# Kernel optimization log

Measured on AMD Instinct MI355X. Metric: run time of the kernel, lower is better.

The kernel has to match this reference:

```python
import jax, jax.numpy as jnp
import numpy as np

N, E, B, T, F, H, O = 50000, 800000, 16, 4, 128, 128, 128
LEAKY = 0.2  # PyG GATConv negative_slope default


def setup_inputs() -> dict:
    key = jax.random.key(0)
    ks = jax.random.split(key, 12)
    s = 0.05
    return {
        "x": jax.random.normal(ks[0], (T, N, F), jnp.float32),
        "edge_index": jax.random.randint(ks[1], (2, E), 0, N, dtype=jnp.int32),
        "batch_idx": jnp.sort(jax.random.randint(ks[2], (N,), 0, B, dtype=jnp.int32)),
        "W1": jax.random.normal(ks[3], (F, H), jnp.float32) * s,
        "att_src1": jax.random.normal(ks[4], (H,), jnp.float32) * s,
        "att_dst1": jax.random.normal(ks[5], (H,), jnp.float32) * s,
        "b1": jnp.zeros((H,), jnp.float32),
        "W2": jax.random.normal(ks[6], (H, O), jnp.float32) * s,
        "att_src2": jax.random.normal(ks[7], (O,), jnp.float32) * s,
        "att_dst2": jax.random.normal(ks[8], (O,), jnp.float32) * s,
        "b2": jnp.zeros((O,), jnp.float32),
    }


def gat_layer(h, src, dst, W, a_src, a_dst, b):
    # PyG GATConv, heads=1, concat=False, self-loops already appended.
    h = h @ W                                  # [N, out]
    alpha_s = h @ a_src                        # [N]
    alpha_d = h @ a_dst                        # [N]
    e = alpha_s[src] + alpha_d[dst]            # [E']
    e = jnp.where(e > 0, e, LEAKY * e)         # leaky_relu
    # softmax over incoming edges of each destination node (every node has a self-loop)
    m = jax.ops.segment_max(e, dst, num_segments=N)
    ex = jnp.exp(e - m[dst])
    z = jax.ops.segment_sum(ex, dst, num_segments=N)
    alpha = ex / z[dst]                        # [E']
    out = jax.ops.segment_sum(alpha[:, None] * h[src], dst, num_segments=N)
    return out + b


def reference(x, edge_index, batch_idx, W1, att_src1, att_dst1, b1, W2, att_src2, att_dst2, b2):
    loops = jnp.arange(N, dtype=edge_index.dtype)
    src = jnp.concatenate([edge_index[0], loops])  # add_self_loops (PyG default)
    dst = jnp.concatenate([edge_index[1], loops])
    ones = jnp.ones((N, 1), jnp.float32)
    cnt = jax.ops.segment_sum(ones, batch_idx, num_segments=B)  # [B,1]

    def per_snapshot(xt):
        h = gat_layer(xt, src, dst, W1, att_src1, att_dst1, b1)
        h = jax.nn.relu(h)                     # inter-layer ReLU (dropout=0, eval)
        h = gat_layer(h, src, dst, W2, att_src2, att_dst2, b2)
        return jax.ops.segment_sum(h, batch_idx, num_segments=B) / cnt  # mean pool [B,O]

    reps = jax.vmap(per_snapshot)(x)           # [T, B, O]
    return jnp.transpose(reps, (1, 0, 2))      # [B, T, O]
```

## Files before the change

kernel.cpp:

```cpp
#include <hip/hip_runtime.h>
#include <hip/hip_bf16.h>

#define LEAKY 0.2f

typedef __attribute__((ext_vector_type(8))) short bf16x8;
typedef __attribute__((ext_vector_type(4))) float f32x4;
typedef __attribute__((ext_vector_type(2))) float f32x2;


__global__ __launch_bounds__(256) void k_init(int* cnt, int* bstart, int* hist, int n, int nb) {
    int i = blockIdx.x * 256 + threadIdx.x;
    if (i < n) cnt[i] = 1;
    if (i < nb) bstart[i] = n;
    if (i < 32) hist[i] = 0;
}

__global__ __launch_bounds__(256) void k_count(const int* __restrict__ dst, int* cnt, int e,
                                               const int* __restrict__ bidx, int* bstart, int n) {
    int i = blockIdx.x * 256 + threadIdx.x;
    if (i < e) atomicAdd(&cnt[dst[i]], 1);
    if (i < n) {
        int b = bidx[i];
        if (i == 0 || bidx[i - 1] != b) atomicMin(&bstart[b], i);
    }
}

__device__ inline int block_incl_scan(int v, int* lds) {
    int lane = threadIdx.x & 63, wid = threadIdx.x >> 6;
    int s = v;
#pragma unroll
    for (int o = 1; o < 64; o <<= 1) { int t = __shfl_up(s, o); if (lane >= o) s += t; }
    if (lane == 63) lds[wid] = s;
    __syncthreads();
    int add = 0;
#pragma unroll
    for (int ww = 0; ww < 3; ++ww) if (ww < wid) add += lds[ww];
    return s + add;
}

__global__ __launch_bounds__(256) void k_scanA(const int* __restrict__ cnt, int* bsum, int n) {
    __shared__ int lds[4];
    int i = blockIdx.x * 256 + threadIdx.x;
    int v = (i < n) ? ((cnt[i] + 15) & ~15) : 0;
    int s = block_incl_scan(v, lds);
    if (threadIdx.x == 255) bsum[blockIdx.x] = s;
}

__global__ __launch_bounds__(256) void k_scanB(int* bsum, int* boff, int nb,
                                               int* bstart, int n, int nbatch) {
    __shared__ int lds[4];
    int i = threadIdx.x;
    int v = (i < nb) ? bsum[i] : 0;
    int s = block_incl_scan(v, lds);
    if (i < nb) boff[i] = s - v;
    if (i == 0) {
        bstart[nbatch] = n;
        for (int b = nbatch - 1; b >= 0; --b)
            if (bstart[b] == n) bstart[b] = bstart[b + 1];
    }
}

__global__ __launch_bounds__(256) void k_scanC(const int* __restrict__ cnt, const int* __restrict__ boff,
                                               int* row_ptr, int* csr, int* cursor, int* hist, int n) {
    __shared__ int lds[4];
    __shared__ int lh[32];
    int tid = threadIdx.x;
    if (tid < 32) lh[tid] = 0;
    int i = blockIdx.x * 256 + tid;
    int v = (i < n) ? ((cnt[i] + 15) & ~15) : 0;
    int s = block_incl_scan(v, lds) + boff[blockIdx.x];
    __syncthreads();
    if (i < n) {
        int excl = s - v;
        row_ptr[i + 1] = s;
        csr[excl] = i;
        cursor[i] = excl + 1;
        atomicAdd(&lh[min(v >> 4, 31)], 1);
    }
    if (i == 0) row_ptr[0] = 0;
    __syncthreads();
    if (tid < 32 && lh[tid]) atomicAdd(&hist[tid], lh[tid]);
}

__global__ __launch_bounds__(256) void k_scatter(const int* __restrict__ src, const int* __restrict__ dst,
                                                 int* cursor, int* csr, int e) {
    int i = blockIdx.x * 256 + threadIdx.x;
    if (i < e) { int p = atomicAdd(&cursor[dst[i]], 1); csr[p] = src[i]; }
}

__global__ void k_bscan(const int* __restrict__ hist, int* bcur) {
    int run = 0;
    for (int b = 0; b < 32; ++b) { bcur[b] = run; run += hist[b]; }
}

__global__ __launch_bounds__(256) void k_pad(const int* __restrict__ row_ptr, const int* __restrict__ cursor,
                                             int* csr, int* bcur, int* perm, int n) {
    __shared__ int lh[32];
    __shared__ int lbase[32];
    int tid = threadIdx.x;
    if (tid < 32) lh[tid] = 0;
    __syncthreads();
    int i = blockIdx.x * 256 + tid;
    int bkt = 0, lpos = 0, b0 = 0, p = 0, e = 0;
    if (i < n) {
        b0 = row_ptr[i]; p = cursor[i]; e = row_ptr[i + 1];
        bkt = min((e - b0) >> 4, 31);
        lpos = atomicAdd(&lh[bkt], 1);
    }
    __syncthreads();
    if (tid < 32 && lh[tid]) lbase[tid] = atomicAdd(&bcur[tid], lh[tid]);
    __syncthreads();
    if (i < n) {
        perm[lbase[bkt] + lpos] = i;
        int v = i | 0x80000000;
        for (; p < e; ++p) csr[p] = v;
    }
}

__device__ inline unsigned short bf16r(float x) {
    unsigned int u = __float_as_uint(x);
    u += 0x7fffu + ((u >> 16) & 1u);
    return (unsigned short)(u >> 16);
}

__device__ inline unsigned int bfpair(float lo, float hi) {
    unsigned int ul = __float_as_uint(lo); ul += 0x7fffu + ((ul >> 16) & 1u);
    unsigned int uh = __float_as_uint(hi); uh += 0x7fffu + ((uh >> 16) & 1u);
    return (ul >> 16) | (uh & 0xffff0000u);
}

__global__ __launch_bounds__(256) void k_prep(const float* __restrict__ W, unsigned short* __restrict__ wtg) {
    int idx = blockIdx.x * 256 + threadIdx.x;
    int k = idx >> 7, n = idx & 127;
    int kg = k >> 3, kr = k & 7;
    wtg[(n * 16 + (kg ^ (n & 15))) * 8 + kr] = bf16r(W[k * 128 + n]);
}

template <bool ABF16>
__global__ __launch_bounds__(256) void k_gemm_mfma(
    const void* __restrict__ Asrc, const unsigned short* __restrict__ wtg,
    const float* __restrict__ asrc, const float* __restrict__ adst,
    unsigned char* __restrict__ hq, float* __restrict__ vas, float* __restrict__ vad,
    int nrows)
{
    __shared__ unsigned short Wt[128 * 128];
    int tid = threadIdx.x;
    int lane = tid & 63, wv = tid >> 6;
    int row0 = blockIdx.x * 128;
    int c0 = lane & 15, g = lane >> 4;

    {
        const uint4* s4 = (const uint4*)wtg;
        uint4* d4 = (uint4*)Wt;
#pragma unroll
        for (int i = 0; i < 8; ++i)
            d4[tid + i * 256] = s4[tid + i * 256];
    }
    __syncthreads();

    f32x4 acc[2][8];
#pragma unroll
    for (int mi = 0; mi < 2; ++mi)
#pragma unroll
        for (int ni = 0; ni < 8; ++ni)
#pragma unroll
            for (int q = 0; q < 4; ++q) acc[mi][ni][q] = 0.f;

    int rA[2];
#pragma unroll
    for (int mi = 0; mi < 2; ++mi)
        rA[mi] = min(row0 + wv * 32 + mi * 16 + c0, nrows - 1);

#pragma unroll
    for (int ks = 0; ks < 4; ++ks) {
        int k0 = ks * 32;
        int kgbase = k0 >> 3;
        bf16x8 af[2];
#pragma unroll
        for (int mi = 0; mi < 2; ++mi) {
            if (ABF16) {
                af[mi] = *(const bf16x8*)((const unsigned short*)Asrc + (size_t)rA[mi] * 128 + k0 + g * 8);
            } else {
                const float4* ap = (const float4*)((const float*)Asrc + (size_t)rA[mi] * 128 + k0 + g * 8);
                float4 f0 = ap[0], f1 = ap[1];
                uint4 p = make_uint4(bfpair(f0.x, f0.y), bfpair(f0.z, f0.w),
                                     bfpair(f1.x, f1.y), bfpair(f1.z, f1.w));
                af[mi] = *(bf16x8*)&p;
            }
        }
        bf16x8 bfr[8];
#pragma unroll
        for (int ni = 0; ni < 8; ++ni) {
            int n = ni * 16 + c0;
            bfr[ni] = *(const bf16x8*)&Wt[(n * 16 + ((kgbase + g) ^ c0)) * 8];
        }
#pragma unroll
        for (int mi = 0; mi < 2; ++mi)
#pragma unroll
            for (int ni = 0; ni < 8; ++ni)
                acc[mi][ni] = __builtin_amdgcn_mfma_f32_16x16x32_bf16(bfr[ni], af[mi], acc[mi][ni], 0, 0, 0);
    }

    float4 as4[8], ad4[8];
#pragma unroll
    for (int ni = 0; ni < 8; ++ni) {
        as4[ni] = *(const float4*)&asrc[ni * 16 + g * 4];
        ad4[ni] = *(const float4*)&adst[ni * 16 + g * 4];
    }
#pragma unroll
    for (int mi = 0; mi < 2; ++mi) {
        int node = row0 + wv * 32 + mi * 16 + c0;
        bool ok = node < nrows;
        float s = 0.f, d = 0.f;
        unsigned packs[8];
#pragma unroll
        for (int ni = 0; ni < 8; ++ni) {
            f32x4 vv = acc[mi][ni];
            s = fmaf(vv[0], as4[ni].x, fmaf(vv[1], as4[ni].y, fmaf(vv[2], as4[ni].z, fmaf(vv[3], as4[ni].w, s))));
            d = fmaf(vv[0], ad4[ni].x, fmaf(vv[1], ad4[ni].y, fmaf(vv[2], ad4[ni].z, fmaf(vv[3], ad4[ni].w, d))));
            unsigned p0 = (unsigned)__builtin_amdgcn_cvt_pk_fp8_f32(vv[0], vv[1], 0, false);
            packs[ni] = (unsigned)__builtin_amdgcn_cvt_pk_fp8_f32(vv[2], vv[3], (int)p0, true);
        }
        s += __shfl_xor(s, 16); s += __shfl_xor(s, 32);
        d += __shfl_xor(d, 16); d += __shfl_xor(d, 32);
        if (ok) {
            if (g == 0) { vas[node] = s; vad[node] = d; }
#pragma unroll
            for (int ni = 0; ni < 8; ++ni)
                *(unsigned*)&hq[(size_t)node * 128 + ni * 16 + g * 4] = packs[ni];
        }
    }
}

template <bool RELU>
__global__ __launch_bounds__(256) void k_agg(const unsigned char* __restrict__ hq,
                                             const float* __restrict__ vas,
                                             const float* __restrict__ vad,
                                             const int* __restrict__ row_ptr,
                                             const int* __restrict__ csr,
                                             const int* __restrict__ perm,
                                             const float* __restrict__ bias,
                                             unsigned int* __restrict__ outb,
                                             int n, int chunksPerT) {
    int i = blockIdx.x;
    int slot = i & 7;
    int t = slot >> 1;
    int chunk = ((i >> 3) << 1) | (slot & 1);
    if (chunk >= chunksPerT) return;
    int tid = threadIdx.x;
    int grp = tid >> 4, l = tid & 15;
    int idx = chunk * 16 + grp;
    if (idx >= n) return;
    int w = perm[idx];
    unsigned int tbase = (unsigned int)t * (unsigned int)n;
    unsigned int g = tbase + (unsigned int)w;
    int beg = row_ptr[w], end = row_ptr[w + 1];
    float advl = vad[g];

    f32x2 acc2[4];
#pragma unroll
    for (int q = 0; q < 4; ++q) { acc2[q].x = 0.f; acc2[q].y = 0.f; }
    float zp = 0.f;

    for (int c = beg; c < end; c += 16) {
        int raw = csr[c + l];
        unsigned int s_l = tbase + (unsigned int)(raw & 0x7fffffff);
        float e = vas[s_l] + advl;
        e = e > 0.f ? e : LEAKY * e;
        float w_l = (raw >= 0) ? __expf(e) : 0.f;
        zp += w_l;

        unsigned int ofs[16]; float wt[16];
#pragma unroll
        for (int q = 0; q < 16; ++q) {
            ofs[q] = __shfl(s_l, q, 16) * 128u + (unsigned int)(l * 8);
            wt[q] = __shfl(w_l, q, 16);
        }
        uint2 v[16];
#pragma unroll
        for (int q = 0; q < 16; ++q)
            v[q] = *(const uint2*)&hq[ofs[q]];
#pragma unroll
        for (int q = 0; q < 16; ++q) {
            f32x2 w2; w2.x = wt[q]; w2.y = wt[q];
            acc2[0] = __builtin_elementwise_fma(w2, __builtin_amdgcn_cvt_pk_f32_fp8(v[q].x, false), acc2[0]);
            acc2[1] = __builtin_elementwise_fma(w2, __builtin_amdgcn_cvt_pk_f32_fp8(v[q].x, true),  acc2[1]);
            acc2[2] = __builtin_elementwise_fma(w2, __builtin_amdgcn_cvt_pk_f32_fp8(v[q].y, false), acc2[2]);
            acc2[3] = __builtin_elementwise_fma(w2, __builtin_amdgcn_cvt_pk_f32_fp8(v[q].y, true),  acc2[3]);
        }
    }

    float z = zp;
#pragma unroll
    for (int o = 1; o < 16; o <<= 1) z += __shfl_xor(z, o, 16);
    float inv = 1.0f / z;

    float4 b0 = *(const float4*)&bias[l * 8];
    float4 b1 = *(const float4*)&bias[l * 8 + 4];
    float4 o0 = make_float4(fmaf(acc2[0].x, inv, b0.x), fmaf(acc2[0].y, inv, b0.y),
                            fmaf(acc2[1].x, inv, b0.z), fmaf(acc2[1].y, inv, b0.w));
    float4 o1 = make_float4(fmaf(acc2[2].x, inv, b1.x), fmaf(acc2[2].y, inv, b1.y),
                            fmaf(acc2[3].x, inv, b1.z), fmaf(acc2[3].y, inv, b1.w));
    if (RELU) {
        o0.x = fmaxf(o0.x, 0.f); o0.y = fmaxf(o0.y, 0.f); o0.z = fmaxf(o0.z, 0.f); o0.w = fmaxf(o0.w, 0.f);
        o1.x = fmaxf(o1.x, 0.f); o1.y = fmaxf(o1.y, 0.f); o1.z = fmaxf(o1.z, 0.f); o1.w = fmaxf(o1.w, 0.f);
    }
    uint4 p = make_uint4(bfpair(o0.x, o0.y), bfpair(o0.z, o0.w),
                         bfpair(o1.x, o1.y), bfpair(o1.z, o1.w));
    *(uint4*)&outb[(size_t)g * 64 + l * 4] = p;
}

__global__ __launch_bounds__(128) void k_pool(const unsigned int* __restrict__ h,
                                              const int* __restrict__ bstart,
                                              float* __restrict__ out, int n, int T) {
    int b = blockIdx.x;
    int chunk = blockIdx.y;
    int t = blockIdx.z;
    int f = threadIdx.x;
    int s = bstart[b], e = bstart[b + 1];
    int cnt = e - s;
    if (cnt <= 0) return;
    int len = (cnt + 31) / 32;
    int cs = s + chunk * len;
    int ce = min(cs + len, e);
    if (cs >= ce) return;
    const unsigned int* ht = h + (size_t)t * n * 64;
    float acc = 0.f;
    for (int nidx = cs; nidx < ce; ++nidx) {
        unsigned int v = ht[(size_t)nidx * 64 + (f >> 1)];
        acc += __uint_as_float((f & 1) ? (v & 0xffff0000u) : (v << 16));
    }
    atomicAdd(&out[(size_t)(b * T + t) * 128 + f], acc / (float)cnt);
}


extern "C" void kernel_launch(void* const* d_in, const int* in_sizes, int n_in,
                              void* d_out, int out_size, void* d_ws, size_t ws_size,
                              hipStream_t stream) {
    const float* x    = (const float*)d_in[0];
    const int*   ei   = (const int*)d_in[1];
    const int*   bidx = (const int*)d_in[2];
    const float* W1   = (const float*)d_in[3];
    const float* as1  = (const float*)d_in[4];
    const float* ad1  = (const float*)d_in[5];
    const float* b1   = (const float*)d_in[6];
    const float* W2   = (const float*)d_in[7];
    const float* as2  = (const float*)d_in[8];
    const float* ad2  = (const float*)d_in[9];
    const float* b2   = (const float*)d_in[10];
    float* out = (float*)d_out;

    const int E = in_sizes[1] / 2;
    const int N = in_sizes[2];
    const int T = in_sizes[0] / (N * 128);
    const int B = out_size / (T * 128);
    const int* src = ei;
    const int* dst = ei + E;
    const int NT = N * T;

    char* wsp = (char*)d_ws;
    auto alloc = [&](size_t bytes) { void* p = wsp; wsp += (bytes + 255) / 256 * 256; return p; };
    unsigned char* hq    = (unsigned char*)alloc((size_t)NT * 128);
    unsigned int* hb2    = (unsigned int*)alloc((size_t)NT * 64 * 4);
    float* vas           = (float*)alloc((size_t)NT * 4);
    float* vad           = (float*)alloc((size_t)NT * 4);
    unsigned short* wt1g = (unsigned short*)alloc(128 * 128 * 2);
    unsigned short* wt2g = (unsigned short*)alloc(128 * 128 * 2);
    int* row_ptr         = (int*)alloc((size_t)(N + 1) * 4);
    int* cnt             = (int*)alloc((size_t)N * 4);
    int* csr             = (int*)alloc(((size_t)E + 16ull * N + 64) * 4);
    int* perm            = (int*)alloc((size_t)N * 4);
    int* hist            = (int*)alloc(32 * 4);
    int* bcur            = (int*)alloc(32 * 4);
    int* bstart          = (int*)alloc((size_t)(B + 2) * 4);
    int  nScanB          = (N + 255) / 256;
    int* bsum            = (int*)alloc((size_t)nScanB * 4);
    int* boff            = (int*)alloc((size_t)nScanB * 4);

    hipMemsetAsync(d_out, 0, (size_t)out_size * sizeof(float), stream);

    int gN = (N + 255) / 256, gE = (E + 255) / 256;
    k_init<<<gN, 256, 0, stream>>>(cnt, bstart, hist, N, B + 1);
    k_count<<<gE, 256, 0, stream>>>(dst, cnt, E, bidx, bstart, N);
    k_prep<<<64, 256, 0, stream>>>(W1, wt1g);
    k_prep<<<64, 256, 0, stream>>>(W2, wt2g);
    k_scanA<<<nScanB, 256, 0, stream>>>(cnt, bsum, N);
    k_scanB<<<1, 256, 0, stream>>>(bsum, boff, nScanB, bstart, N, B);
    k_scanC<<<nScanB, 256, 0, stream>>>(cnt, boff, row_ptr, csr, cnt, hist, N);
    k_scatter<<<gE, 256, 0, stream>>>(src, dst, cnt, csr, E);
    k_bscan<<<1, 1, 0, stream>>>(hist, bcur);
    k_pad<<<gN, 256, 0, stream>>>(row_ptr, cnt, csr, bcur, perm, N);

    int gGemm = (NT + 127) / 128;
    int chunksPerT = (N + 15) / 16;
    int chunksPad = ((chunksPerT + 1) / 2) * 2;
    int gAggFlat = chunksPad * 4;
    k_gemm_mfma<false><<<gGemm, 256, 0, stream>>>(x,   wt1g, as1, ad1, hq, vas, vad, NT);
    k_agg<true ><<<gAggFlat, 256, 0, stream>>>(hq, vas, vad, row_ptr, csr, perm, b1, hb2, N, chunksPerT);
    k_gemm_mfma<true ><<<gGemm, 256, 0, stream>>>(hb2, wt2g, as2, ad2, hq, vas, vad, NT);
    k_agg<false><<<gAggFlat, 256, 0, stream>>>(hq, vas, vad, row_ptr, csr, perm, b2, hb2, N, chunksPerT);
    k_pool<<<dim3(B, 32, T), 128, 0, stream>>>(hb2, bstart, out, N, T);
}
```

Measured before the change: 332.2 us.

## Use 8-lane groups per node with 16-byte gathers and padding to 8

The aggregation kernel now gives each destination node 8 lanes instead of 16, with each lane loading 16 fp8 features (uint4) per neighbor, so a 256-thread block covers 32 nodes. CSR row padding and degree buckets move from multiples of 16 to multiples of 8, which cuts wasted padded-edge work for low-degree nodes (average degree is about 17). The cost is more registers per lane (16 accumulators) and twice as many edge-loop iterations per node, which may lower occupancy.

After: 328.2 us. No clear change (-1.2%).

```diff
diff --git a/kernel.cpp b/kernel.cpp
--- a/kernel.cpp
+++ b/kernel.cpp
@@ -41,7 +41,7 @@
 __global__ __launch_bounds__(256) void k_scanA(const int* __restrict__ cnt, int* bsum, int n) {
     __shared__ int lds[4];
     int i = blockIdx.x * 256 + threadIdx.x;
-    int v = (i < n) ? ((cnt[i] + 15) & ~15) : 0;
+    int v = (i < n) ? ((cnt[i] + 7) & ~7) : 0;
     int s = block_incl_scan(v, lds);
     if (threadIdx.x == 255) bsum[blockIdx.x] = s;
 }
@@ -67,7 +67,7 @@
     int tid = threadIdx.x;
     if (tid < 32) lh[tid] = 0;
     int i = blockIdx.x * 256 + tid;
-    int v = (i < n) ? ((cnt[i] + 15) & ~15) : 0;
+    int v = (i < n) ? ((cnt[i] + 7) & ~7) : 0;
     int s = block_incl_scan(v, lds) + boff[blockIdx.x];
     __syncthreads();
     if (i < n) {
@@ -75,7 +75,7 @@
         row_ptr[i + 1] = s;
         csr[excl] = i;
         cursor[i] = excl + 1;
-        atomicAdd(&lh[min(v >> 4, 31)], 1);
+        atomicAdd(&lh[min(v >> 3, 31)], 1);
     }
     if (i == 0) row_ptr[0] = 0;
     __syncthreads();
@@ -104,7 +104,7 @@
     int bkt = 0, lpos = 0, b0 = 0, p = 0, e = 0;
     if (i < n) {
         b0 = row_ptr[i]; p = cursor[i]; e = row_ptr[i + 1];
-        bkt = min((e - b0) >> 4, 31);
+        bkt = min((e - b0) >> 3, 31);
         lpos = atomicAdd(&lh[bkt], 1);
     }
     __syncthreads();
@@ -248,8 +248,8 @@
     int chunk = ((i >> 3) << 1) | (slot & 1);
     if (chunk >= chunksPerT) return;
     int tid = threadIdx.x;
-    int grp = tid >> 4, l = tid & 15;
-    int idx = chunk * 16 + grp;
+    int grp = tid >> 3, l = tid & 7;
+    int idx = chunk * 32 + grp;
     if (idx >= n) return;
     int w = perm[idx];
     unsigned int tbase = (unsigned int)t * (unsigned int)n;
@@ -257,12 +257,12 @@
     int beg = row_ptr[w], end = row_ptr[w + 1];
     float advl = vad[g];
 
-    f32x2 acc2[4];
-#pragma unroll
-    for (int q = 0; q < 4; ++q) { acc2[q].x = 0.f; acc2[q].y = 0.f; }
+    f32x2 acc2[8];
+#pragma unroll
+    for (int q = 0; q < 8; ++q) { acc2[q].x = 0.f; acc2[q].y = 0.f; }
     float zp = 0.f;
 
-    for (int c = beg; c < end; c += 16) {
+    for (int c = beg; c < end; c += 8) {
         int raw = csr[c + l];
         unsigned int s_l = tbase + (unsigned int)(raw & 0x7fffffff);
         float e = vas[s_l] + advl;
@@ -270,44 +270,53 @@
         float w_l = (raw >= 0) ? __expf(e) : 0.f;
         zp += w_l;
 
-        unsigned int ofs[16]; float wt[16];
-#pragma unroll
-        for (int q = 0; q < 16; ++q) {
-            ofs[q] = __shfl(s_l, q, 16) * 128u + (unsigned int)(l * 8);
-            wt[q] = __shfl(w_l, q, 16);
-        }
-        uint2 v[16];
-#pragma unroll
-        for (int q = 0; q < 16; ++q)
-            v[q] = *(const uint2*)&hq[ofs[q]];
-#pragma unroll
-        for (int q = 0; q < 16; ++q) {
+        unsigned int ofs[8]; float wt[8];
+#pragma unroll
+        for (int q = 0; q < 8; ++q) {
+            ofs[q] = __shfl(s_l, q, 8) * 128u + (unsigned int)(l * 16);
+            wt[q] = __shfl(w_l, q, 8);
+        }
+        uint4 v[8];
+#pragma unroll
+        for (int q = 0; q < 8; ++q)
+            v[q] = *(const uint4*)&hq[ofs[q]];
+#pragma unroll
+        for (int q = 0; q < 8; ++q) {
             f32x2 w2; w2.x = wt[q]; w2.y = wt[q];
             acc2[0] = __builtin_elementwise_fma(w2, __builtin_amdgcn_cvt_pk_f32_fp8(v[q].x, false), acc2[0]);
             acc2[1] = __builtin_elementwise_fma(w2, __builtin_amdgcn_cvt_pk_f32_fp8(v[q].x, true),  acc2[1]);
             acc2[2] = __builtin_elementwise_fma(w2, __builtin_amdgcn_cvt_pk_f32_fp8(v[q].y, false), acc2[2]);
             acc2[3] = __builtin_elementwise_fma(w2, __builtin_amdgcn_cvt_pk_f32_fp8(v[q].y, true),  acc2[3]);
+            acc2[4] = __builtin_elementwise_fma(w2, __builtin_amdgcn_cvt_pk_f32_fp8(v[q].z, false), acc2[4]);
+            acc2[5] = __builtin_elementwise_fma(w2, __builtin_amdgcn_cvt_pk_f32_fp8(v[q].z, true),  acc2[5]);
+            acc2[6] = __builtin_elementwise_fma(w2, __builtin_amdgcn_cvt_pk_f32_fp8(v[q].w, false), acc2[6]);
+            acc2[7] = __builtin_elementwise_fma(w2, __builtin_amdgcn_cvt_pk_f32_fp8(v[q].w, true),  acc2[7]);
         }
     }
 
     float z = zp;
-#pragma unroll
-    for (int o = 1; o < 16; o <<= 1) z += __shfl_xor(z, o, 16);
+    z += __shfl_xor(z, 1, 8);
+    z += __shfl_xor(z, 2, 8);
+    z += __shfl_xor(z, 4, 8);
     float inv = 1.0f / z;
 
-    float4 b0 = *(const float4*)&bias[l * 8];
-    float4 b1 = *(const float4*)&bias[l * 8 + 4];
-    float4 o0 = make_float4(fmaf(acc2[0].x, inv, b0.x), fmaf(acc2[0].y, inv, b0.y),
-                            fmaf(acc2[1].x, inv, b0.z), fmaf(acc2[1].y, inv, b0.w));
-    float4 o1 = make_float4(fmaf(acc2[2].x, inv, b1.x), fmaf(acc2[2].y, inv, b1.y),
-                            fmaf(acc2[3].x, inv, b1.z), fmaf(acc2[3].y, inv, b1.w));
-    if (RELU) {
-        o0.x = fmaxf(o0.x, 0.f); o0.y = fmaxf(o0.y, 0.f); o0.z = fmaxf(o0.z, 0.f); o0.w = fmaxf(o0.w, 0.f);
-        o1.x = fmaxf(o1.x, 0.f); o1.y = fmaxf(o1.y, 0.f); o1.z = fmaxf(o1.z, 0.f); o1.w = fmaxf(o1.w, 0.f);
-    }
-    uint4 p = make_uint4(bfpair(o0.x, o0.y), bfpair(o0.z, o0.w),
-                         bfpair(o1.x, o1.y), bfpair(o1.z, o1.w));
-    *(uint4*)&outb[(size_t)g * 64 + l * 4] = p;
+    const float4* bias4 = (const float4*)&bias[l * 16];
+    unsigned u[8];
+#pragma unroll
+    for (int j = 0; j < 4; ++j) {
+        float4 bb = bias4[j];
+        float o0 = fmaf(acc2[2 * j].x, inv, bb.x);
+        float o1 = fmaf(acc2[2 * j].y, inv, bb.y);
+        float o2 = fmaf(acc2[2 * j + 1].x, inv, bb.z);
+        float o3 = fmaf(acc2[2 * j + 1].y, inv, bb.w);
+        if (RELU) {
+            o0 = fmaxf(o0, 0.f); o1 = fmaxf(o1, 0.f); o2 = fmaxf(o2, 0.f); o3 = fmaxf(o3, 0.f);
+        }
+        u[2 * j]     = bfpair(o0, o1);
+        u[2 * j + 1] = bfpair(o2, o3);
+    }
+    *(uint4*)&outb[(size_t)g * 64 + l * 8]     = make_uint4(u[0], u[1], u[2], u[3]);
+    *(uint4*)&outb[(size_t)g * 64 + l * 8 + 4] = make_uint4(u[4], u[5], u[6], u[7]);
 }
 
 __global__ __launch_bounds__(128) void k_pool(const unsigned int* __restrict__ h,
@@ -392,7 +401,7 @@
     k_pad<<<gN, 256, 0, stream>>>(row_ptr, cnt, csr, bcur, perm, N);
 
     int gGemm = (NT + 127) / 128;
-    int chunksPerT = (N + 15) / 16;
+    int chunksPerT = (N + 31) / 32;
     int chunksPad = ((chunksPerT + 1) / 2) * 2;
     int gAggFlat = chunksPad * 4;
     k_gemm_mfma<false><<<gGemm, 256, 0, stream>>>(x,   wt1g, as1, ad1, hq, vas, vad, NT);
```
